# Performance work log

Hardware: AMD Instinct MI355X
Metric: run time of the kernel (lower is better)

## Reference

```python
import jax, jax.numpy as jnp
import numpy as np
from jax import lax

EPS = float(np.finfo(np.float64).eps)  # matches np.finfo(float).eps in torch module
C, K = 32, 128   # coarse_num, event_num
B, T, TP = 4, 512, 1024


def _fine_probs(cf_logits, ftc):
    # p(fine k | coarse c(k)) : softmax of logits restricted to each coarse group
    e = jnp.exp(cf_logits - jnp.max(cf_logits))            # [K]
    denom = jax.ops.segment_sum(e, ftc, num_segments=C)    # [C]
    return e / denom[ftc]                                  # [K]


def setup_inputs() -> dict:
    key = jax.random.key(0)
    ks = jax.random.split(key, 7)
    past_event = jax.random.randint(ks[0], (B, T), 0, C)                     # coarse ids of past events
    dt = jax.random.uniform(ks[1], (B, T), minval=0.0, maxval=0.1)
    past_time = jnp.cumsum(dt, axis=-1).astype(jnp.float32)                  # increasing event times
    horizon = float(T) * 0.05
    time_tensor = jax.random.uniform(ks[2], (B, TP), minval=0.0, maxval=horizon).astype(jnp.float32)
    mu = 0.1 * jax.random.normal(ks[3], (C,), dtype=jnp.float32)
    alpha = 0.1 * jax.random.normal(ks[4], (C, C), dtype=jnp.float32)
    delta = 0.1 * jax.random.normal(ks[5], (C, C), dtype=jnp.float32)
    cf_logits = 0.1 * jax.random.normal(ks[6], (K,), dtype=jnp.float32)
    ftc = jnp.arange(K) % C                                                   # fine -> coarse map
    return dict(past_event=past_event, past_time=past_time, time_tensor=time_tensor,
                mu=mu, alpha=alpha, delta=delta, cf_logits=cf_logits, ftc=ftc)


def reference(past_event, past_time, time_tensor, mu, alpha, delta, cf_logits, ftc):
    Bb, Tp = time_tensor.shape
    Cc = mu.shape[0]
    past_alpha = jax.nn.softplus(alpha)[past_event]          # [B,T,C]
    past_delta = jax.nn.softplus(delta)[past_event] + EPS    # [B,T,C]

    def step(acc, xs):
        pa_i, pd_i, pt_i = xs                                # [B,C],[B,C],[B]
        et = time_tensor - pt_i[:, None]                     # [B,Tp]
        use = (et > EPS).astype(acc.dtype)                   # causal mask
        etc = jnp.where(et < EPS, 0.0, et)
        effect = pa_i[:, None, :] * jnp.exp(-pd_i[:, None, :] * etc[:, :, None])  # [B,Tp,C]
        return acc + effect * use[:, :, None], None

    acc0 = jnp.zeros((Bb, Tp, Cc), dtype=time_tensor.dtype)
    acc, _ = lax.scan(step, acc0,
                      (past_alpha.transpose(1, 0, 2), past_delta.transpose(1, 0, 2), past_time.T))
    all_inten = acc + jax.nn.softplus(mu)[None, None, :]     # [B,Tp,C]
    fine_inten = all_inten[..., ftc] * _fine_probs(cf_logits, ftc)  # [B,Tp,K]
    return fine_inten
```

## Files before the change

### kernel.cpp

```cpp
#include <hip/hip_runtime.h>

#define BB   4
#define TT   512
#define TPN  1024
#define CC   32
#define KK   128
#define EPSF 2.220446049250313e-16f
#define LOG2E 1.4426950408889634f

#if __has_builtin(__builtin_amdgcn_exp2f)
#define EXP2F(x) __builtin_amdgcn_exp2f(x)
#else
#define EXP2F(x) exp2f(x)
#endif

__device__ __forceinline__ float softplus_f(float x) {
    return fmaxf(x, 0.f) + log1pf(__expf(-fabsf(x)));
}

__global__ __launch_bounds__(256, 8) void GHP_fused(
    const int*   __restrict__ past_event,
    const float* __restrict__ past_time,
    const float* __restrict__ time_tensor,
    const float* __restrict__ mu,
    const float* __restrict__ alpha,
    const float* __restrict__ delta,
    const float* __restrict__ cf_logits,
    const int*   __restrict__ ftc,
    float*       __restrict__ out)
{
    __shared__ __align__(16) float2 sad_s[CC * CC];
    __shared__ __align__(16) float2 ptev_s[4 * 128];
    __shared__ float e_s[KK];
    __shared__ int   ftc_s[KK];
    __shared__ float den_s[CC];
    __shared__ float spmu_s[CC];
    __shared__ float part_s[2 * 4 * CC];

    const int tid = threadIdx.x;
    const int b   = blockIdx.x >> 9;
    const int tp0 = (blockIdx.x & 511) << 1;

    #pragma unroll
    for (int idx = tid; idx < CC * CC; idx += 256) {
        const float a = softplus_f(alpha[idx]);
        const float d = (softplus_f(delta[idx]) + EPSF) * LOG2E;
        sad_s[idx] = make_float2(a, d);
    }
    #pragma unroll
    for (int i = tid; i < TT; i += 256) {
        const int r = i & 3, j = i >> 2;
        ptev_s[(r << 7) + j] = make_float2(past_time[b * TT + i],
                                           __int_as_float(past_event[b * TT + i] << 5));
    }
    if (tid < KK) {
        e_s[tid] = __expf(cf_logits[tid]);
        ftc_s[tid] = ftc[tid];
    }
    if (tid < CC) {
        den_s[tid]  = 0.f;
        spmu_s[tid] = softplus_f(mu[tid]);
    }
    __syncthreads();
    if (tid < KK) atomicAdd(&den_s[ftc_s[tid]], e_s[tid]);

    const int c   = tid & 31;
    const int h   = (tid >> 5) & 1;
    const int w   = (tid >> 6) & 1;
    const int tpl = tid >> 7;
    const int r   = (w << 1) + h;
    const float t = time_tensor[b * TPN + tp0 + tpl];

    const float2* pp = ptev_s + (r << 7);
    int lo = 0, hi = 128;
    #pragma unroll
    for (int s = 0; s < 8; ++s) {
        const int mid = (lo + hi) >> 1;
        const bool go = (lo < hi) && ((t - pp[mid].x) > EPSF);
        lo = go ? mid + 1 : lo;
        hi = go ? hi : mid;
    }
    const int J = lo;

    float acc0 = 0.f, acc1 = 0.f;
    int j = 0;
    #pragma unroll 2
    for (; j + 4 <= J; j += 4) {
        const float4 q0 = *(const float4*)(pp + j);
        const float4 q1 = *(const float4*)(pp + j + 2);
        const float2 ad0 = sad_s[__float_as_int(q0.y) + c];
        const float2 ad1 = sad_s[__float_as_int(q0.w) + c];
        const float2 ad2 = sad_s[__float_as_int(q1.y) + c];
        const float2 ad3 = sad_s[__float_as_int(q1.w) + c];
        acc0 = fmaf(ad0.x, EXP2F(-ad0.y * (t - q0.x)), acc0);
        acc1 = fmaf(ad1.x, EXP2F(-ad1.y * (t - q0.z)), acc1);
        acc0 = fmaf(ad2.x, EXP2F(-ad2.y * (t - q1.x)), acc0);
        acc1 = fmaf(ad3.x, EXP2F(-ad3.y * (t - q1.z)), acc1);
    }
    for (; j < J; ++j) {
        const float2 pe = pp[j];
        const float2 ad = sad_s[__float_as_int(pe.y) + c];
        acc0 = fmaf(ad.x, EXP2F(-ad.y * (t - pe.x)), acc0);
    }
    part_s[((tpl << 2) + r) * CC + c] = acc0 + acc1;
    __syncthreads();

    {
        const int k   = tid & 127;
        const int tpe = tid >> 7;
        const int ck  = ftc_s[k];
        const float* ps = part_s + (tpe << 7);
        const float inten = ((ps[ck] + ps[CC + ck]) + (ps[2 * CC + ck] + ps[3 * CC + ck]))
                            + spmu_s[ck];
        const float p = e_s[k] / den_s[ck];
        out[(size_t)(b * TPN + tp0 + tpe) * KK + k] = inten * p;
    }
}

extern "C" void kernel_launch(void* const* d_in, const int* in_sizes, int n_in,
                              void* d_out, int out_size, void* d_ws, size_t ws_size,
                              hipStream_t stream) {
    const int*   past_event  = (const int*)  d_in[0];
    const float* past_time   = (const float*)d_in[1];
    const float* time_tensor = (const float*)d_in[2];
    const float* mu          = (const float*)d_in[3];
    const float* alpha       = (const float*)d_in[4];
    const float* delta       = (const float*)d_in[5];
    const float* cf_logits   = (const float*)d_in[6];
    const int*   ftc         = (const int*)  d_in[7];
    float*       out         = (float*)d_out;

    GHP_fused<<<BB * (TPN / 2), 256, 0, stream>>>(past_event, past_time, time_tensor,
                                                  mu, alpha, delta, cf_logits, ftc, out);
}
```

Baseline: 87.32 us.

## Process two coarse channels per thread with packed f32x2 math, split events eight ways

Each thread now handles two adjacent coarse channels using 2-wide float vectors, which lets the compiler emit packed FMA/mul instructions. The alpha and negated delta tables are split into separate packed arrays. The past events are split into eight strided subsets instead of four, so the binary search is shorter and the per-thread loop is halved. The final reduction now sums eight partials instead of four. The exp2 count per thread is unchanged, so the gain depends on packed-math throughput and less duplicated event and index loading.

```diff
diff --git a/kernel.cpp b/kernel.cpp
--- a/kernel.cpp
+++ b/kernel.cpp
@@ -14,6 +14,8 @@
 #define EXP2F(x) exp2f(x)
 #endif
 
+typedef float f32x2 __attribute__((ext_vector_type(2)));
+
 __device__ __forceinline__ float softplus_f(float x) {
     return fmaxf(x, 0.f) + log1pf(__expf(-fabsf(x)));
 }
@@ -29,13 +31,14 @@
     const int*   __restrict__ ftc,
     float*       __restrict__ out)
 {
-    __shared__ __align__(16) float2 sad_s[CC * CC];
-    __shared__ __align__(16) float2 ptev_s[4 * 128];
+    __shared__ __align__(16) f32x2 nd2_s[CC * CC / 2];
+    __shared__ __align__(16) f32x2 a2_s[CC * CC / 2];
+    __shared__ __align__(16) float2 ptev_s[8 * 64];
     __shared__ float e_s[KK];
     __shared__ int   ftc_s[KK];
     __shared__ float den_s[CC];
     __shared__ float spmu_s[CC];
-    __shared__ float part_s[2 * 4 * CC];
+    __shared__ __align__(16) f32x2 part2_s[2 * 8 * 16];
 
     const int tid = threadIdx.x;
     const int b   = blockIdx.x >> 9;
@@ -43,15 +46,14 @@
 
     #pragma unroll
     for (int idx = tid; idx < CC * CC; idx += 256) {
-        const float a = softplus_f(alpha[idx]);
-        const float d = (softplus_f(delta[idx]) + EPSF) * LOG2E;
-        sad_s[idx] = make_float2(a, d);
+        ((float*)a2_s)[idx]  = softplus_f(alpha[idx]);
+        ((float*)nd2_s)[idx] = -(softplus_f(delta[idx]) + EPSF) * LOG2E;
     }
     #pragma unroll
     for (int i = tid; i < TT; i += 256) {
-        const int r = i & 3, j = i >> 2;
-        ptev_s[(r << 7) + j] = make_float2(past_time[b * TT + i],
-                                           __int_as_float(past_event[b * TT + i] << 5));
+        const int r = i & 7, j = i >> 3;
+        ptev_s[(r << 6) + j] = make_float2(past_time[b * TT + i],
+                                           __int_as_float(past_event[b * TT + i] << 4));
     }
     if (tid < KK) {
         e_s[tid] = __expf(cf_logits[tid]);
@@ -64,17 +66,15 @@
     __syncthreads();
     if (tid < KK) atomicAdd(&den_s[ftc_s[tid]], e_s[tid]);
 
-    const int c   = tid & 31;
-    const int h   = (tid >> 5) & 1;
-    const int w   = (tid >> 6) & 1;
+    const int c   = tid & 15;
+    const int r   = (tid >> 4) & 7;
     const int tpl = tid >> 7;
-    const int r   = (w << 1) + h;
     const float t = time_tensor[b * TPN + tp0 + tpl];
 
-    const float2* pp = ptev_s + (r << 7);
-    int lo = 0, hi = 128;
+    const float2* pp = ptev_s + (r << 6);
+    int lo = 0, hi = 64;
     #pragma unroll
-    for (int s = 0; s < 8; ++s) {
+    for (int s = 0; s < 7; ++s) {
         const int mid = (lo + hi) >> 1;
         const bool go = (lo < hi) && ((t - pp[mid].x) > EPSF);
         lo = go ? mid + 1 : lo;
@@ -82,36 +82,43 @@
     }
     const int J = lo;
 
-    float acc0 = 0.f, acc1 = 0.f;
+    f32x2 acc0 = {0.f, 0.f}, acc1 = {0.f, 0.f};
     int j = 0;
     #pragma unroll 2
-    for (; j + 4 <= J; j += 4) {
-        const float4 q0 = *(const float4*)(pp + j);
-        const float4 q1 = *(const float4*)(pp + j + 2);
-        const float2 ad0 = sad_s[__float_as_int(q0.y) + c];
-        const float2 ad1 = sad_s[__float_as_int(q0.w) + c];
-        const float2 ad2 = sad_s[__float_as_int(q1.y) + c];
-        const float2 ad3 = sad_s[__float_as_int(q1.w) + c];
-        acc0 = fmaf(ad0.x, EXP2F(-ad0.y * (t - q0.x)), acc0);
-        acc1 = fmaf(ad1.x, EXP2F(-ad1.y * (t - q0.z)), acc1);
-        acc0 = fmaf(ad2.x, EXP2F(-ad2.y * (t - q1.x)), acc0);
-        acc1 = fmaf(ad3.x, EXP2F(-ad3.y * (t - q1.z)), acc1);
+    for (; j + 2 <= J; j += 2) {
+        const float4 q = *(const float4*)(pp + j);
+        const int i0 = __float_as_int(q.y) + c;
+        const int i1 = __float_as_int(q.w) + c;
+        const f32x2 nd0 = nd2_s[i0], aa0 = a2_s[i0];
+        const f32x2 nd1 = nd2_s[i1], aa1 = a2_s[i1];
+        const float et0 = t - q.x;
+        const float et1 = t - q.z;
+        const f32x2 g0 = nd0 * et0;
+        const f32x2 g1 = nd1 * et1;
+        const f32x2 ex0 = {EXP2F(g0.x), EXP2F(g0.y)};
+        const f32x2 ex1 = {EXP2F(g1.x), EXP2F(g1.y)};
+        acc0 += aa0 * ex0;
+        acc1 += aa1 * ex1;
     }
-    for (; j < J; ++j) {
+    if (j < J) {
         const float2 pe = pp[j];
-        const float2 ad = sad_s[__float_as_int(pe.y) + c];
-        acc0 = fmaf(ad.x, EXP2F(-ad.y * (t - pe.x)), acc0);
+        const int i0 = __float_as_int(pe.y) + c;
+        const f32x2 nd0 = nd2_s[i0], aa0 = a2_s[i0];
+        const f32x2 g0 = nd0 * (t - pe.x);
+        const f32x2 ex0 = {EXP2F(g0.x), EXP2F(g0.y)};
+        acc0 += aa0 * ex0;
     }
-    part_s[((tpl << 2) + r) * CC + c] = acc0 + acc1;
+    part2_s[((tpl << 3) + r) * 16 + c] = acc0 + acc1;
     __syncthreads();
 
     {
         const int k   = tid & 127;
         const int tpe = tid >> 7;
         const int ck  = ftc_s[k];
-        const float* ps = part_s + (tpe << 7);
-        const float inten = ((ps[ck] + ps[CC + ck]) + (ps[2 * CC + ck] + ps[3 * CC + ck]))
-                            + spmu_s[ck];
+        const float* ps = (const float*)(part2_s + (tpe << 7));
+        float inten = spmu_s[ck];
+        #pragma unroll
+        for (int rr = 0; rr < 8; ++rr) inten += ps[rr * CC + ck];
         const float p = e_s[k] / den_s[ck];
         out[(size_t)(b * TPN + tp0 + tpe) * KK + k] = inten * p;
     }
```

Measured after the change: 87.64 us. Within noise of the previous version (+0.4%).
